# Kernel tuning notes

Hardware: AMD Instinct MI355X
Metric: run time of the kernel (lower is better)

Reference implementation:

```python
import jax, jax.numpy as jnp
import numpy as np
from jax import lax

N = 2048
B = 8
CH = 10
START = 1
STOP = 65


def setup_inputs() -> dict:
    key = jax.random.key(0)
    ks = jax.random.split(key, 13)

    def g(k, s):
        return jax.random.normal(k, s, jnp.float32) * 0.05

    return {
        "x": jax.random.normal(ks[0], (B, 1, N, N), jnp.float32),
        "wl": g(ks[1], (CH // 2, 1, 3, N)), "bl": g(ks[2], (CH // 2,)),
        "wr": g(ks[3], (CH // 2, 1, N, 3)), "br": g(ks[4], (CH // 2,)),
        "wA": g(ks[5], (CH, CH, 3)), "bA": g(ks[6], (CH,)),
        "wB": g(ks[7], (CH, CH, 3)), "bB": g(ks[8], (CH,)),  # shared by layers 2&3 (torch list aliasing)
        "wT": g(ks[9], (CH, CH, 3)), "bT": g(ks[10], (CH,)),
        "wm": g(ks[11], (2, CH, 1)), "bm": g(ks[12], (2,)),
        "start": START, "stop": STOP,
    }


def _conv1d(h, w, b, pad):
    y = lax.conv_general_dilated(h, w, (1,), [(pad, pad)], dimension_numbers=("NCH", "OIH", "NCH"))
    return y + b[None, :, None]


def _forward(x, wl, bl, wr, br, wA, bA, wB, bB, wT, bT, wm, bm, start, stop):
    n = x.shape[-1]
    # scan_left: Conv2d kernel (3, n), padding (1, 0) -> (B, 5, n, 1) -> squeeze
    left_ = lax.conv_general_dilated(x, wl, (1, 1), [(1, 1), (0, 0)], dimension_numbers=("NCHW", "OIHW", "NCHW"))
    left_ = left_[..., 0] + bl[None, :, None]
    # scan_right: Conv2d kernel (n, 3), padding (0, 1) -> (B, 5, 1, n) -> squeeze
    right_ = lax.conv_general_dilated(x, wr, (1, 1), [(0, 0), (1, 1)], dimension_numbers=("NCHW", "OIHW", "NCHW"))
    right_ = right_[:, :, 0, :] + br[None, :, None]
    lr = jnp.concatenate([left_, right_], axis=1)  # (B, 10, n)
    h = jax.nn.relu(_conv1d(lr, wA, bA, 1))
    h = jax.nn.relu(_conv1d(h, wB, bB, 1))  # same weights twice: torch [conv, relu]*2 aliasing
    h = jax.nn.relu(_conv1d(h, wB, bB, 1))
    # ConvTranspose1d(k=3, stride=1, pad=1) == Conv1d with transposed, spatially-flipped kernel, pad=1
    wTc = jnp.flip(jnp.swapaxes(wT, 0, 1), -1)
    for _ in range(3):
        h = jax.nn.relu(_conv1d(h, wTc, bT, 1))
    m = jax.nn.sigmoid(_conv1d(h, wm, bm, 0))  # (B, 2, n)
    left, right = m[:, 0, :], m[:, 1, :]
    xs = x[:, 0]  # (B, n, n)
    preds = []
    for d in range(start, stop):  # static diagonal indices
        curr = jnp.exp(jnp.diagonal(xs, offset=d, axis1=1, axis2=2))  # (B, n-d)
        mass_in = curr[:, 1:] * right[:, 1:n - d] + curr[:, :-1] * left[:, d:n - 1]
        mass_out = right[:, 0:n - d - 1] + left[:, d + 1:n]
        p = jnp.log(mass_in / mass_out)
        preds.append(p - jnp.mean(p))  # scalar mean over batch+positions, as torch.mean
    return jnp.concatenate(preds, axis=1)  # ragged preds concatenated: (B, sum(n-d-1))


def reference(x, wl, bl, wr, br, wA, bA, wB, bB, wT, bT, wm, bm, start, stop):
    return _forward(x, wl, bl, wr, br, wA, bA, wB, bB, wT, bT, wm, bm, start, stop)
```

## Files before the change

### kernel.cpp

```cpp
#include <hip/hip_runtime.h>
#include <hip/hip_bf16.h>

#define NN 2048
#define BB 8
#define TROW 128928

typedef __attribute__((ext_vector_type(8))) short bf16x8;
typedef __attribute__((ext_vector_type(4))) float f32x4;

__device__ __forceinline__ short f2bf(float f) {
    unsigned u = __float_as_uint(f);
    unsigned r = (u + 0x7FFFu + ((u >> 16) & 1u)) >> 16;
    return (short)r;
}

__global__ __launch_bounds__(256) void k_stage1(const float* __restrict__ x,
                                                const float* __restrict__ wl,
                                                const float* __restrict__ wr,
                                                float* __restrict__ Rp,
                                                float* __restrict__ CSp,
                                                float* __restrict__ psum,
                                                int* __restrict__ counter) {
    int blk = blockIdx.x;
    int tid = threadIdx.x;
    if (blk == 0 && tid < 65) {
        if (tid < 64) psum[tid] = 0.f;
        else *counter = 0;
    }
    if (blk < 1024) {
        int b = blk >> 7;
        int sub = blk & 127;
        int rg = sub >> 2, ks = sub & 3;
        int wv = tid >> 6, lane = tid & 63;
        int q = lane >> 4, m = lane & 15;
        int r0 = rg * 64 + wv * 16;
        int nrow = (m == 15) ? 14 : m;
        int k0 = ks * 512 + q * 8;

        const float* ap = x + ((size_t)(b * NN + r0 + m)) * NN + k0;
        const float* bp = wl + (size_t)nrow * NN + k0;

        f32x4 acc = {0.f, 0.f, 0.f, 0.f};
#pragma unroll 4
        for (int it = 0; it < 16; it++) {
            const float* a0 = ap + it * 32;
            const float* b0 = bp + it * 32;
            float4 av0 = *(const float4*)(a0);
            float4 av1 = *(const float4*)(a0 + 4);
            float4 bv0 = *(const float4*)(b0);
            float4 bv1 = *(const float4*)(b0 + 4);
            bf16x8 af, bf;
            af[0] = f2bf(av0.x); af[1] = f2bf(av0.y); af[2] = f2bf(av0.z); af[3] = f2bf(av0.w);
            af[4] = f2bf(av1.x); af[5] = f2bf(av1.y); af[6] = f2bf(av1.z); af[7] = f2bf(av1.w);
            bf[0] = f2bf(bv0.x); bf[1] = f2bf(bv0.y); bf[2] = f2bf(bv0.z); bf[3] = f2bf(bv0.w);
            bf[4] = f2bf(bv1.x); bf[5] = f2bf(bv1.y); bf[6] = f2bf(bv1.z); bf[7] = f2bf(bv1.w);
            acc = __builtin_amdgcn_mfma_f32_16x16x32_bf16(af, bf, acc, 0, 0, 0);
        }
        float* rp = Rp + (size_t)ks * 262144 + ((size_t)b * NN + r0) * 16;
#pragma unroll
        for (int reg = 0; reg < 4; reg++)
            rp[(q * 4 + reg) * 16 + m] = acc[reg];
    } else {
        int blk2 = blk - 1024;
        int b = blk2 >> 5;
        int rem = blk2 & 31;
        int jc = rem >> 4, rc = rem & 15;
        int r0 = rc * 128;
        int c0 = jc * 1024 + tid * 4;
        const float* xp = x + ((size_t)b * NN + r0) * NN + c0;

        float acc[15][4];
#pragma unroll
        for (int k = 0; k < 15; k++)
#pragma unroll
            for (int e = 0; e < 4; e++) acc[k][e] = 0.f;

        for (int rb = 0; rb < 16; rb++) {
            float4 xv[8];
#pragma unroll
            for (int q = 0; q < 8; q++)
                xv[q] = *(const float4*)(xp + (size_t)(rb * 8 + q) * NN);
#pragma unroll
            for (int q = 0; q < 8; q++) {
                int h = r0 + rb * 8 + q;
#pragma unroll
                for (int k = 0; k < 15; k++) {
                    int c = k / 3, dw = k - c * 3;
                    float wk = wr[c * (NN * 3) + h * 3 + dw];
                    acc[k][0] = fmaf(xv[q].x, wk, acc[k][0]);
                    acc[k][1] = fmaf(xv[q].y, wk, acc[k][1]);
                    acc[k][2] = fmaf(xv[q].z, wk, acc[k][2]);
                    acc[k][3] = fmaf(xv[q].w, wk, acc[k][3]);
                }
            }
        }
        float* outp = CSp + ((size_t)(rc * BB + b) * 16) * NN + c0;
#pragma unroll
        for (int k = 0; k < 15; k++) {
            float4 v; v.x = acc[k][0]; v.y = acc[k][1]; v.z = acc[k][2]; v.w = acc[k][3];
            *(float4*)(outp + (size_t)k * NN) = v;
        }
    }
}

__global__ __launch_bounds__(256) void k_csum(const float* __restrict__ CSp,
                                              float* __restrict__ CS,
                                              const float* __restrict__ Rp,
                                              float* __restrict__ R) {
    int blk = blockIdx.x;
    if (blk < 256) {
        int vid = blk * 256 + threadIdx.x;
        const float4* src = (const float4*)CSp;
        float4 s = src[vid];
#pragma unroll
        for (int rc = 1; rc < 16; rc++) {
            float4 v = src[vid + rc * 65536];
            s.x += v.x; s.y += v.y; s.z += v.z; s.w += v.w;
        }
        ((float4*)CS)[vid] = s;
    } else {
        int vid = (blk - 256) * 256 + threadIdx.x;
        const float4* src = (const float4*)Rp;
        float4 s = src[vid];
#pragma unroll
        for (int ks = 1; ks < 4; ks++) {
            float4 v = src[vid + ks * 65536];
            s.x += v.x; s.y += v.y; s.z += v.z; s.w += v.w;
        }
        ((float4*)R)[vid] = s;
    }
}

__global__ __launch_bounds__(256) void k_chainC(const float* __restrict__ R,
                                                const float* __restrict__ CS,
                                                const float* __restrict__ bl,
                                                const float* __restrict__ br,
                                                const float* __restrict__ wA, const float* __restrict__ bA,
                                                const float* __restrict__ wB, const float* __restrict__ bB,
                                                const float* __restrict__ wT, const float* __restrict__ bT,
                                                const float* __restrict__ wm, const float* __restrict__ bm,
                                                float* __restrict__ LEFT, float* __restrict__ RIGHT) {
    __shared__ float buf0[10][144], buf1[10][144];
    __shared__ float W[3][10][10][3];
    __shared__ float Bs[3][10];
    __shared__ float Wm[2][10], Bm[2];
    int b = blockIdx.x >> 4;
    int c0 = (blockIdx.x & 15) << 7;
    int tid = threadIdx.x;

    for (int idx = tid; idx < 900; idx += 256) {
        int set = idx / 300, rem = idx - set * 300;
        int o = rem / 30, rem2 = rem - o * 30, c = rem2 / 3, kk = rem2 - c * 3;
        float u;
        if (set == 0) u = wA[o * 30 + c * 3 + kk];
        else if (set == 1) u = wB[o * 30 + c * 3 + kk];
        else u = wT[c * 30 + o * 3 + (2 - kk)];
        W[set][o][c][kk] = u;
    }
    if (tid < 30) {
        float v = (tid < 10) ? bA[tid] : (tid < 20) ? bB[tid - 10] : bT[tid - 20];
        Bs[tid / 10][tid % 10] = v;
    }
    if (tid < 20) Wm[tid / 10][tid % 10] = wm[tid];
    if (tid < 2) Bm[tid] = bm[tid];

    for (int idx = tid; idx < 1400; idx += 256) {
        int ch = idx / 140, p = idx - ch * 140;
        int g = c0 - 6 + p;
        float v = 0.f;
        if (g >= 0 && g < NN) {
            if (ch < 5) {
                v = bl[ch];
#pragma unroll
                for (int dh = 0; dh < 3; dh++) {
                    int r = g + dh - 1;
                    if (r >= 0 && r < NN) v += R[(size_t)(b * NN + r) * 16 + ch * 3 + dh];
                }
            } else {
                int c = ch - 5;
                v = br[c];
#pragma unroll
                for (int dw = 0; dw < 3; dw++) {
                    int j = g + dw - 1;
                    if (j >= 0 && j < NN)
                        v += CS[((size_t)b * 16 + c * 3 + dw) * NN + j];
                }
            }
        }
        buf0[ch][p] = v;
    }
    __syncthreads();

    float(*in)[144] = buf0;
    float(*out)[144] = buf1;
    for (int layer = 0; layer < 6; layer++) {
        int set = (layer == 0) ? 0 : (layer < 3 ? 1 : 2);
        int lo = layer + 1;
        for (int idx = tid; idx < 1400; idx += 256) {
            int o = idx / 140, p = idx - o * 140;
            if (p >= lo && p < 140 - lo) {
                float s = Bs[set][o];
#pragma unroll
                for (int c = 0; c < 10; c++) {
                    const float* ip = &in[c][p];
                    s = fmaf(ip[-1], W[set][o][c][0], s);
                    s = fmaf(ip[0], W[set][o][c][1], s);
                    s = fmaf(ip[1], W[set][o][c][2], s);
                }
                s = s > 0.f ? s : 0.f;
                int g = c0 - 6 + p;
                if (g < 0 || g >= NN) s = 0.f;
                out[o][p] = s;
            }
        }
        __syncthreads();
        float(*tmp)[144] = in; in = out; out = tmp;
    }
    {
        int idx = tid;
        int o = idx >> 7, pp = idx & 127;
        int p = 6 + pp;
        float s = Bm[o];
#pragma unroll
        for (int c = 0; c < 10; c++) s = fmaf(in[c][p], Wm[o][c], s);
        float sig = 1.f / (1.f + __expf(-s));
        (o ? RIGHT : LEFT)[b * NN + c0 + pp] = sig;
    }
}

__global__ __launch_bounds__(256) void k_diagout(const float* __restrict__ x,
                                                 const float* __restrict__ LEFT,
                                                 const float* __restrict__ RIGHT,
                                                 float* __restrict__ psum,
                                                 int* __restrict__ counter,
                                                 float* __restrict__ outp) {
    __shared__ float T[65][65];
    __shared__ float psl[64];
    int b = blockIdx.x >> 5;
    int i0 = (blockIdx.x & 31) << 6;
    int tid = threadIdx.x;

    for (int idx = tid; idx < 65 * 64; idx += 256) {
        int r = idx >> 6, dm1 = idx & 63;
        int row = i0 + r;
        int col = row + dm1 + 1;
        float v = 0.f;
        if (row < NN && col < NN) v = __expf(x[((size_t)b * NN + row) * NN + col]);
        T[r][dm1] = v;
    }
    __syncthreads();

    int wv = tid >> 6, lane = tid & 63;
    int i = i0 + lane;
    const float* lf = LEFT + b * NN;
    const float* rt = RIGHT + b * NN;
    float pv[16];
#pragma unroll
    for (int s = 0; s < 16; s++) {
        int dm1 = wv * 16 + s;
        int d = dm1 + 1;
        int L = (NN - 1) - d;
        float p = 0.f;
        if (i < L) {
            float mi = T[lane + 1][dm1] * rt[i + 1] + T[lane][dm1] * lf[d + i];
            float mo = rt[i] + lf[d + 1 + i];
            p = __logf(mi / mo);
        }
        pv[s] = p;
        float s64 = p;
        for (int off = 32; off; off >>= 1) s64 += __shfl_down(s64, off);
        if (lane == 0) psl[dm1] = s64;
    }
    __syncthreads();
    if (tid < 64) atomicAdd(&psum[tid], psl[tid]);
    __syncthreads();
    if (tid == 0) {
        __threadfence();
        atomicAdd(counter, 1);
        while (__hip_atomic_load(counter, __ATOMIC_ACQUIRE, __HIP_MEMORY_SCOPE_AGENT) < 256) {}
    }
    __syncthreads();
    if (tid < 64)
        psl[tid] = __hip_atomic_load(&psum[tid], __ATOMIC_RELAXED, __HIP_MEMORY_SCOPE_AGENT);
    __syncthreads();

#pragma unroll
    for (int s = 0; s < 16; s++) {
        int dm1 = wv * 16 + s;
        int d = dm1 + 1;
        int L = (NN - 1) - d;
        if (i < L) {
            float mean = psl[dm1] / (float)(8 * L);
            size_t off0 = (size_t)dm1 * (NN - 1) - (size_t)dm1 * (dm1 + 1) / 2;
            outp[(size_t)b * TROW + off0 + i] = pv[s] - mean;
        }
    }
}

extern "C" void kernel_launch(void* const* d_in, const int* in_sizes, int n_in,
                              void* d_out, int out_size, void* d_ws, size_t ws_size,
                              hipStream_t stream) {
    const float* x = (const float*)d_in[0];
    const float* wl = (const float*)d_in[1];
    const float* bl = (const float*)d_in[2];
    const float* wr = (const float*)d_in[3];
    const float* br = (const float*)d_in[4];
    const float* wA = (const float*)d_in[5];
    const float* bA = (const float*)d_in[6];
    const float* wB = (const float*)d_in[7];
    const float* bB = (const float*)d_in[8];
    const float* wT = (const float*)d_in[9];
    const float* bT = (const float*)d_in[10];
    const float* wm = (const float*)d_in[11];
    const float* bm = (const float*)d_in[12];

    float* ws = (float*)d_ws;
    float* R    = ws;
    float* Rp   = ws + 262144;
    float* CSp  = ws + 1310720;
    float* CS   = ws + 5505024;
    float* LEFT = ws + 5767168;
    float* RIGHT= ws + 5783552;
    float* psum = ws + 5799936;
    int*   counter = (int*)(ws + 5800000);

    k_stage1<<<1280, 256, 0, stream>>>(x, wl, wr, Rp, CSp, psum, counter);
    k_csum<<<512, 256, 0, stream>>>(CSp, CS, Rp, R);
    k_chainC<<<128, 256, 0, stream>>>(R, CS, bl, br, wA, bA, wB, bB, wT, bT, wm, bm, LEFT, RIGHT);
    k_diagout<<<256, 256, 0, stream>>>(x, LEFT, RIGHT, psum, counter, (float*)d_out);
}
```

Measured before the change: 296.0 us.

## Fuse partial-sum reduction, conv chain and diagonal output into one kernel

Removes the separate k_csum reduction kernel by having the conv-chain blocks sum the split-K and row-chunk partials directly while gathering their inputs. The chain and diagonal-output stages are merged into one 384-block launch. Diagonal blocks preload their exp(x) tiles, then spin on an atomic counter until all chain blocks have published LEFT/RIGHT. This cuts two launches and the intermediate R/CS round trip to memory. The cost is redundant partial-sum reads in the chain blocks, and the spin-wait depends on all 384 blocks being resident at once or on chain blocks being scheduled first.

```diff
diff --git a/kernel.cpp b/kernel.cpp
--- a/kernel.cpp
+++ b/kernel.cpp
@@ -20,12 +20,12 @@
                                                 float* __restrict__ Rp,
                                                 float* __restrict__ CSp,
                                                 float* __restrict__ psum,
-                                                int* __restrict__ counter) {
+                                                int* __restrict__ counters) {
     int blk = blockIdx.x;
     int tid = threadIdx.x;
-    if (blk == 0 && tid < 65) {
+    if (blk == 0 && tid < 66) {
         if (tid < 64) psum[tid] = 0.f;
-        else *counter = 0;
+        else counters[tid - 64] = 0;
     }
     if (blk < 1024) {
         int b = blk >> 7;
@@ -103,196 +103,193 @@
     }
 }
 
-__global__ __launch_bounds__(256) void k_csum(const float* __restrict__ CSp,
-                                              float* __restrict__ CS,
+union SMem {
+    struct {
+        float buf0[10][144], buf1[10][144];
+        float W[3][10][10][3];
+        float Bs[3][10];
+        float Wm[2][10], Bm[2];
+    } ch;
+    struct {
+        float T[65][65];
+        float psl[64];
+    } dg;
+};
+
+__global__ __launch_bounds__(256) void k_tail(const float* __restrict__ x,
                                               const float* __restrict__ Rp,
-                                              float* __restrict__ R) {
+                                              const float* __restrict__ CSp,
+                                              const float* __restrict__ bl,
+                                              const float* __restrict__ br,
+                                              const float* __restrict__ wA, const float* __restrict__ bA,
+                                              const float* __restrict__ wB, const float* __restrict__ bB,
+                                              const float* __restrict__ wT, const float* __restrict__ bT,
+                                              const float* __restrict__ wm, const float* __restrict__ bm,
+                                              float* __restrict__ LEFT, float* __restrict__ RIGHT,
+                                              float* __restrict__ psum,
+                                              int* __restrict__ counters,
+                                              float* __restrict__ outp) {
+    __shared__ SMem sm;
     int blk = blockIdx.x;
-    if (blk < 256) {
-        int vid = blk * 256 + threadIdx.x;
-        const float4* src = (const float4*)CSp;
-        float4 s = src[vid];
-#pragma unroll
-        for (int rc = 1; rc < 16; rc++) {
-            float4 v = src[vid + rc * 65536];
-            s.x += v.x; s.y += v.y; s.z += v.z; s.w += v.w;
-        }
-        ((float4*)CS)[vid] = s;
+    int tid = threadIdx.x;
+
+    if (blk < 128) {
+        int b = blk >> 4;
+        int c0 = (blk & 15) << 7;
+
+        for (int idx = tid; idx < 900; idx += 256) {
+            int set = idx / 300, rem = idx - set * 300;
+            int o = rem / 30, rem2 = rem - o * 30, c = rem2 / 3, kk = rem2 - c * 3;
+            float u;
+            if (set == 0) u = wA[o * 30 + c * 3 + kk];
+            else if (set == 1) u = wB[o * 30 + c * 3 + kk];
+            else u = wT[c * 30 + o * 3 + (2 - kk)];
+            sm.ch.W[set][o][c][kk] = u;
+        }
+        if (tid < 30) {
+            float v = (tid < 10) ? bA[tid] : (tid < 20) ? bB[tid - 10] : bT[tid - 20];
+            sm.ch.Bs[tid / 10][tid % 10] = v;
+        }
+        if (tid < 20) sm.ch.Wm[tid / 10][tid % 10] = wm[tid];
+        if (tid < 2) sm.ch.Bm[tid] = bm[tid];
+
+        for (int idx = tid; idx < 1400; idx += 256) {
+            int ch = idx / 140, p = idx - ch * 140;
+            int g = c0 - 6 + p;
+            float v = 0.f;
+            if (g >= 0 && g < NN) {
+                if (ch < 5) {
+                    v = bl[ch];
+#pragma unroll
+                    for (int dh = 0; dh < 3; dh++) {
+                        int r = g + dh - 1;
+                        if (r >= 0 && r < NN) {
+                            size_t base = ((size_t)b * NN + r) * 16 + ch * 3 + dh;
+#pragma unroll
+                            for (int ks = 0; ks < 4; ks++)
+                                v += Rp[(size_t)ks * 262144 + base];
+                        }
+                    }
+                } else {
+                    int c = ch - 5;
+                    v = br[c];
+#pragma unroll
+                    for (int dw = 0; dw < 3; dw++) {
+                        int j = g + dw - 1;
+                        if (j >= 0 && j < NN) {
+#pragma unroll
+                            for (int rc = 0; rc < 16; rc++)
+                                v += CSp[(((size_t)rc * BB + b) * 16 + c * 3 + dw) * NN + j];
+                        }
+                    }
+                }
+            }
+            sm.ch.buf0[ch][p] = v;
+        }
+        __syncthreads();
+
+        float(*in)[144] = sm.ch.buf0;
+        float(*out)[144] = sm.ch.buf1;
+        for (int layer = 0; layer < 6; layer++) {
+            int set = (layer == 0) ? 0 : (layer < 3 ? 1 : 2);
+            int lo = layer + 1;
+            for (int idx = tid; idx < 1400; idx += 256) {
+                int o = idx / 140, p = idx - o * 140;
+                if (p >= lo && p < 140 - lo) {
+                    float s = sm.ch.Bs[set][o];
+#pragma unroll
+                    for (int c = 0; c < 10; c++) {
+                        const float* ip = &in[c][p];
+                        s = fmaf(ip[-1], sm.ch.W[set][o][c][0], s);
+                        s = fmaf(ip[0], sm.ch.W[set][o][c][1], s);
+                        s = fmaf(ip[1], sm.ch.W[set][o][c][2], s);
+                    }
+                    s = s > 0.f ? s : 0.f;
+                    int g = c0 - 6 + p;
+                    if (g < 0 || g >= NN) s = 0.f;
+                    out[o][p] = s;
+                }
+            }
+            __syncthreads();
+            float(*tmp)[144] = in; in = out; out = tmp;
+        }
+        {
+            int o = tid >> 7, pp = tid & 127;
+            int p = 6 + pp;
+            float s = sm.ch.Bm[o];
+#pragma unroll
+            for (int c = 0; c < 10; c++) s = fmaf(in[c][p], sm.ch.Wm[o][c], s);
+            float sig = 1.f / (1.f + __expf(-s));
+            (o ? RIGHT : LEFT)[b * NN + c0 + pp] = sig;
+        }
+        __syncthreads();
+        if (tid == 0) {
+            __threadfence();
+            atomicAdd(&counters[0], 1);
+        }
     } else {
-        int vid = (blk - 256) * 256 + threadIdx.x;
-        const float4* src = (const float4*)Rp;
-        float4 s = src[vid];
-#pragma unroll
-        for (int ks = 1; ks < 4; ks++) {
-            float4 v = src[vid + ks * 65536];
-            s.x += v.x; s.y += v.y; s.z += v.z; s.w += v.w;
-        }
-        ((float4*)R)[vid] = s;
-    }
-}
-
-__global__ __launch_bounds__(256) void k_chainC(const float* __restrict__ R,
-                                                const float* __restrict__ CS,
-                                                const float* __restrict__ bl,
-                                                const float* __restrict__ br,
-                                                const float* __restrict__ wA, const float* __restrict__ bA,
-                                                const float* __restrict__ wB, const float* __restrict__ bB,
-                                                const float* __restrict__ wT, const float* __restrict__ bT,
-                                                const float* __restrict__ wm, const float* __restrict__ bm,
-                                                float* __restrict__ LEFT, float* __restrict__ RIGHT) {
-    __shared__ float buf0[10][144], buf1[10][144];
-    __shared__ float W[3][10][10][3];
-    __shared__ float Bs[3][10];
-    __shared__ float Wm[2][10], Bm[2];
-    int b = blockIdx.x >> 4;
-    int c0 = (blockIdx.x & 15) << 7;
-    int tid = threadIdx.x;
-
-    for (int idx = tid; idx < 900; idx += 256) {
-        int set = idx / 300, rem = idx - set * 300;
-        int o = rem / 30, rem2 = rem - o * 30, c = rem2 / 3, kk = rem2 - c * 3;
-        float u;
-        if (set == 0) u = wA[o * 30 + c * 3 + kk];
-        else if (set == 1) u = wB[o * 30 + c * 3 + kk];
-        else u = wT[c * 30 + o * 3 + (2 - kk)];
-        W[set][o][c][kk] = u;
-    }
-    if (tid < 30) {
-        float v = (tid < 10) ? bA[tid] : (tid < 20) ? bB[tid - 10] : bT[tid - 20];
-        Bs[tid / 10][tid % 10] = v;
-    }
-    if (tid < 20) Wm[tid / 10][tid % 10] = wm[tid];
-    if (tid < 2) Bm[tid] = bm[tid];
-
-    for (int idx = tid; idx < 1400; idx += 256) {
-        int ch = idx / 140, p = idx - ch * 140;
-        int g = c0 - 6 + p;
-        float v = 0.f;
-        if (g >= 0 && g < NN) {
-            if (ch < 5) {
-                v = bl[ch];
-#pragma unroll
-                for (int dh = 0; dh < 3; dh++) {
-                    int r = g + dh - 1;
-                    if (r >= 0 && r < NN) v += R[(size_t)(b * NN + r) * 16 + ch * 3 + dh];
-                }
-            } else {
-                int c = ch - 5;
-                v = br[c];
-#pragma unroll
-                for (int dw = 0; dw < 3; dw++) {
-                    int j = g + dw - 1;
-                    if (j >= 0 && j < NN)
-                        v += CS[((size_t)b * 16 + c * 3 + dw) * NN + j];
-                }
-            }
-        }
-        buf0[ch][p] = v;
-    }
-    __syncthreads();
-
-    float(*in)[144] = buf0;
-    float(*out)[144] = buf1;
-    for (int layer = 0; layer < 6; layer++) {
-        int set = (layer == 0) ? 0 : (layer < 3 ? 1 : 2);
-        int lo = layer + 1;
-        for (int idx = tid; idx < 1400; idx += 256) {
-            int o = idx / 140, p = idx - o * 140;
-            if (p >= lo && p < 140 - lo) {
-                float s = Bs[set][o];
-#pragma unroll
-                for (int c = 0; c < 10; c++) {
-                    const float* ip = &in[c][p];
-                    s = fmaf(ip[-1], W[set][o][c][0], s);
-                    s = fmaf(ip[0], W[set][o][c][1], s);
-                    s = fmaf(ip[1], W[set][o][c][2], s);
-                }
-                s = s > 0.f ? s : 0.f;
-                int g = c0 - 6 + p;
-                if (g < 0 || g >= NN) s = 0.f;
-                out[o][p] = s;
-            }
-        }
-        __syncthreads();
-        float(*tmp)[144] = in; in = out; out = tmp;
-    }
-    {
-        int idx = tid;
-        int o = idx >> 7, pp = idx & 127;
-        int p = 6 + pp;
-        float s = Bm[o];
-#pragma unroll
-        for (int c = 0; c < 10; c++) s = fmaf(in[c][p], Wm[o][c], s);
-        float sig = 1.f / (1.f + __expf(-s));
-        (o ? RIGHT : LEFT)[b * NN + c0 + pp] = sig;
-    }
-}
-
-__global__ __launch_bounds__(256) void k_diagout(const float* __restrict__ x,
-                                                 const float* __restrict__ LEFT,
-                                                 const float* __restrict__ RIGHT,
-                                                 float* __restrict__ psum,
-                                                 int* __restrict__ counter,
-                                                 float* __restrict__ outp) {
-    __shared__ float T[65][65];
-    __shared__ float psl[64];
-    int b = blockIdx.x >> 5;
-    int i0 = (blockIdx.x & 31) << 6;
-    int tid = threadIdx.x;
-
-    for (int idx = tid; idx < 65 * 64; idx += 256) {
-        int r = idx >> 6, dm1 = idx & 63;
-        int row = i0 + r;
-        int col = row + dm1 + 1;
-        float v = 0.f;
-        if (row < NN && col < NN) v = __expf(x[((size_t)b * NN + row) * NN + col]);
-        T[r][dm1] = v;
-    }
-    __syncthreads();
-
-    int wv = tid >> 6, lane = tid & 63;
-    int i = i0 + lane;
-    const float* lf = LEFT + b * NN;
-    const float* rt = RIGHT + b * NN;
-    float pv[16];
-#pragma unroll
-    for (int s = 0; s < 16; s++) {
-        int dm1 = wv * 16 + s;
-        int d = dm1 + 1;
-        int L = (NN - 1) - d;
-        float p = 0.f;
-        if (i < L) {
-            float mi = T[lane + 1][dm1] * rt[i + 1] + T[lane][dm1] * lf[d + i];
-            float mo = rt[i] + lf[d + 1 + i];
-            p = __logf(mi / mo);
-        }
-        pv[s] = p;
-        float s64 = p;
-        for (int off = 32; off; off >>= 1) s64 += __shfl_down(s64, off);
-        if (lane == 0) psl[dm1] = s64;
-    }
-    __syncthreads();
-    if (tid < 64) atomicAdd(&psum[tid], psl[tid]);
-    __syncthreads();
-    if (tid == 0) {
-        __threadfence();
-        atomicAdd(counter, 1);
-        while (__hip_atomic_load(counter, __ATOMIC_ACQUIRE, __HIP_MEMORY_SCOPE_AGENT) < 256) {}
-    }
-    __syncthreads();
-    if (tid < 64)
-        psl[tid] = __hip_atomic_load(&psum[tid], __ATOMIC_RELAXED, __HIP_MEMORY_SCOPE_AGENT);
-    __syncthreads();
-
-#pragma unroll
-    for (int s = 0; s < 16; s++) {
-        int dm1 = wv * 16 + s;
-        int d = dm1 + 1;
-        int L = (NN - 1) - d;
-        if (i < L) {
-            float mean = psl[dm1] / (float)(8 * L);
-            size_t off0 = (size_t)dm1 * (NN - 1) - (size_t)dm1 * (dm1 + 1) / 2;
-            outp[(size_t)b * TROW + off0 + i] = pv[s] - mean;
+        int blk2 = blk - 128;
+        int b = blk2 >> 5;
+        int i0 = (blk2 & 31) << 6;
+
+        for (int idx = tid; idx < 65 * 64; idx += 256) {
+            int r = idx >> 6, dm1 = idx & 63;
+            int row = i0 + r;
+            int col = row + dm1 + 1;
+            float v = 0.f;
+            if (row < NN && col < NN) v = __expf(x[((size_t)b * NN + row) * NN + col]);
+            sm.dg.T[r][dm1] = v;
+        }
+        __syncthreads();
+        if (tid == 0) {
+            while (__hip_atomic_load(&counters[0], __ATOMIC_ACQUIRE, __HIP_MEMORY_SCOPE_AGENT) < 128) {}
+        }
+        __syncthreads();
+
+        int wv = tid >> 6, lane = tid & 63;
+        int i = i0 + lane;
+        const float* lf = LEFT + b * NN;
+        const float* rt = RIGHT + b * NN;
+        float pv[16];
+#pragma unroll
+        for (int s = 0; s < 16; s++) {
+            int dm1 = wv * 16 + s;
+            int d = dm1 + 1;
+            int L = (NN - 1) - d;
+            float p = 0.f;
+            if (i < L) {
+                float mi = sm.dg.T[lane + 1][dm1] * rt[i + 1] + sm.dg.T[lane][dm1] * lf[d + i];
+                float mo = rt[i] + lf[d + 1 + i];
+                p = __logf(mi / mo);
+            }
+            pv[s] = p;
+            float s64 = p;
+            for (int off = 32; off; off >>= 1) s64 += __shfl_down(s64, off);
+            if (lane == 0) sm.dg.psl[dm1] = s64;
+        }
+        __syncthreads();
+        if (tid < 64) atomicAdd(&psum[tid], sm.dg.psl[tid]);
+        __syncthreads();
+        if (tid == 0) {
+            __threadfence();
+            atomicAdd(&counters[1], 1);
+            while (__hip_atomic_load(&counters[1], __ATOMIC_ACQUIRE, __HIP_MEMORY_SCOPE_AGENT) < 256) {}
+        }
+        __syncthreads();
+        if (tid < 64)
+            sm.dg.psl[tid] = __hip_atomic_load(&psum[tid], __ATOMIC_RELAXED, __HIP_MEMORY_SCOPE_AGENT);
+        __syncthreads();
+
+#pragma unroll
+        for (int s = 0; s < 16; s++) {
+            int dm1 = wv * 16 + s;
+            int d = dm1 + 1;
+            int L = (NN - 1) - d;
+            if (i < L) {
+                float mean = sm.dg.psl[dm1] / (float)(8 * L);
+                size_t off0 = (size_t)dm1 * (NN - 1) - (size_t)dm1 * (dm1 + 1) / 2;
+                outp[(size_t)b * TROW + off0 + i] = pv[s] - mean;
+            }
         }
     }
 }
@@ -315,17 +312,14 @@
     const float* bm = (const float*)d_in[12];
 
     float* ws = (float*)d_ws;
-    float* R    = ws;
-    float* Rp   = ws + 262144;
-    float* CSp  = ws + 1310720;
-    float* CS   = ws + 5505024;
-    float* LEFT = ws + 5767168;
-    float* RIGHT= ws + 5783552;
-    float* psum = ws + 5799936;
-    int*   counter = (int*)(ws + 5800000);
-
-    k_stage1<<<1280, 256, 0, stream>>>(x, wl, wr, Rp, CSp, psum, counter);
-    k_csum<<<512, 256, 0, stream>>>(CSp, CS, Rp, R);
-    k_chainC<<<128, 256, 0, stream>>>(R, CS, bl, br, wA, bA, wB, bB, wT, bT, wm, bm, LEFT, RIGHT);
-    k_diagout<<<256, 256, 0, stream>>>(x, LEFT, RIGHT, psum, counter, (float*)d_out);
+    float* Rp   = ws;
+    float* CSp  = ws + 1048576;
+    float* LEFT = ws + 5242880;
+    float* RIGHT= ws + 5259264;
+    float* psum = ws + 5275648;
+    int*   counters = (int*)(ws + 5275712);
+
+    k_stage1<<<1280, 256, 0, stream>>>(x, wl, wr, Rp, CSp, psum, counters);
+    k_tail<<<384, 256, 0, stream>>>(x, Rp, CSp, bl, br, wA, bA, wB, bB, wT, bT, wm, bm,
+                                    LEFT, RIGHT, psum, counters, (float*)d_out);
 }
```

After: 352.6 us. 19.1% more time.
